# Optimization experiments

Hardware: AMD Instinct MI355X
Metric: run time of the kernel (lower is better)

## Reference

```python
import jax, jax.numpy as jnp
import numpy as np

FACTORS = (16, 8, 8)          # prod == n_embd == 1024
H, DK = 16, 64
FACTOR_PARAMS = tuple(f * (f - 1) // 2 for f in FACTORS)  # (120, 28, 28)
DV = sum(FACTOR_PARAMS)       # 176
DVP = 256                     # next power of two padding
B, T, C = 2, 2048, 1024
OFFSET = 64


def _skew_exp(params, f):
    """params: (..., f*(f-1)//2) -> rotation matrices (..., f, f) via expm of skew-sym."""
    rows, cols = np.triu_indices(f, k=1)
    batch = params.shape[:-1]
    mat = jnp.zeros(batch + (f, f), jnp.float32).at[..., rows, cols].set(params.astype(jnp.float32))
    S = mat - jnp.swapaxes(mat, -1, -2)
    R = jax.vmap(jax.scipy.linalg.expm)(S.reshape((-1, f, f)))
    return R.reshape(batch + (f, f))


def setup_inputs() -> dict:
    key = jax.random.key(0)
    k1, k2, k3, k4, k5 = jax.random.split(key, 5)
    return {
        "x": jax.random.normal(k1, (B, T, C), jnp.float32),
        "cached_k": jax.random.normal(k2, (B, H, OFFSET, DK), jnp.float32),
        "cached_v": jax.random.normal(k3, (B, H, OFFSET, DVP), jnp.float32),
        "W_QK": jax.random.normal(k4, (2 * H * DK, C), jnp.float32) * 0.02,
        "W_V": jax.random.normal(k5, (H * DV, C), jnp.float32) * 0.02,
    }


def reference(x, cached_k, cached_v, W_QK, W_V):
    Bx, Tx, Cx = x.shape
    qk = x @ W_QK.T                                  # (B,T,2*H*DK)
    q, k = jnp.split(qk, 2, axis=-1)
    q = q.reshape(Bx, Tx, H, DK).transpose(0, 2, 1, 3)   # (B,H,T,DK)
    k = k.reshape(Bx, Tx, H, DK).transpose(0, 2, 1, 3)
    v = (x @ W_V.T).reshape(Bx, Tx, H, DV).transpose(0, 2, 1, 3)  # (B,H,T,DV)
    v = jnp.pad(v, ((0, 0), (0, 0), (0, 0), (0, DVP - DV)))       # pad to DVP

    offset = cached_k.shape[2]
    k = jnp.concatenate([cached_k, k], axis=2)       # (B,H,offset+T,DK)
    v = jnp.concatenate([cached_v, v], axis=2)       # (B,H,offset+T,DVP)

    neg_inf = jnp.finfo(jnp.float32).min
    causal = jnp.triu(jnp.full((Tx, Tx), neg_inf, jnp.float32), k=1)
    mask = jnp.concatenate([jnp.zeros((Tx, offset), jnp.float32), causal], axis=1)

    scores = jnp.einsum('bhqd,bhkd->bhqk', q, k) * (1.0 / np.sqrt(DK)) + mask
    attn = jax.nn.softmax(scores, axis=-1)
    rot = jnp.einsum('bhqk,bhkd->bhqd', attn, v)[..., :DV]   # (B,H,T,DV)
    rot = rot.transpose(0, 2, 1, 3).sum(axis=2)              # sum over heads -> (B,T,DV)

    splits = jnp.split(rot, np.cumsum(FACTOR_PARAMS)[:-1].tolist(), axis=-1)
    y = x.reshape(Bx, Tx, *FACTORS)
    for i, (p, f) in enumerate(zip(splits, FACTORS)):
        R = _skew_exp(p, f).astype(x.dtype)          # (B,T,f,f)
        y = jnp.moveaxis(y, 2 + i, 2)
        sh = y.shape
        y = (R @ y.reshape(Bx, Tx, f, -1)).reshape(sh)
        y = jnp.moveaxis(y, 2, 2 + i)
    y = y.reshape(Bx, Tx, Cx)
    return y, k, v
```

## Files before the change

### kernel.cpp

```cpp
#include <hip/hip_runtime.h>

typedef _Float16 h8 __attribute__((ext_vector_type(8)));
typedef _Float16 h4 __attribute__((ext_vector_type(4)));
typedef float f4 __attribute__((ext_vector_type(4)));

#define NB 2
#define NT 2048
#define NC 1024
#define NH 16
#define DKK 64
#define DV 176
#define DVP 256
#define OFF 64
#define KV 2112
#define SCALE_Q 0.18033688011112f
#define CLAMP_S 11.541560327111f

__device__ __forceinline__ void load_lds16(const _Float16* g, _Float16* l) {
    __builtin_amdgcn_global_load_lds(
        (const __attribute__((address_space(1))) void*)g,
        (__attribute__((address_space(3))) void*)l, 16, 0, 0);
}

#define PREPA_X   1048576
#define PREPA_QK  1572864
#define PREPA_WV  2293760
#define PREPA_END 2473984
__global__ __launch_bounds__(256)
void k_prep_a(const float* __restrict__ x, const float* __restrict__ wqk,
              const float* __restrict__ wv, _Float16* __restrict__ xh,
              _Float16* __restrict__ wqkh, _Float16* __restrict__ wvh,
              float* __restrict__ rotb) {
    int i = blockIdx.x * 256 + threadIdx.x;
    if (i >= PREPA_END) return;
    if (i < PREPA_X) {
        float4 v = *(const float4*)(x + (size_t)i * 4);
        h4 h = {(_Float16)v.x, (_Float16)v.y, (_Float16)v.z, (_Float16)v.w};
        *(h4*)(xh + (size_t)i * 4) = h;
    } else if (i < PREPA_QK) {
        int j = i - PREPA_X;
        float4 v = *(const float4*)(wqk + (size_t)j * 4);
        h4 h = {(_Float16)v.x, (_Float16)v.y, (_Float16)v.z, (_Float16)v.w};
        *(h4*)(wqkh + (size_t)j * 4) = h;
    } else if (i < PREPA_WV) {
        int j = i - PREPA_QK;
        float4 v = *(const float4*)(wv + (size_t)j * 4);
        h4 h = {(_Float16)v.x, (_Float16)v.y, (_Float16)v.z, (_Float16)v.w};
        *(h4*)(wvh + (size_t)j * 4) = h;
    } else {
        int j = i - PREPA_WV;
        *(float4*)(rotb + (size_t)j * 4) = (float4){0.f, 0.f, 0.f, 0.f};
    }
}

#define PREPB_CK   32768
#define PREPB_CV   163840
#define PREPB_END  1474560
__global__ __launch_bounds__(256)
void k_prep_b(const float* __restrict__ ck, const float* __restrict__ cv,
              float* __restrict__ out_k, _Float16* __restrict__ kh,
              float* __restrict__ out_v, _Float16* __restrict__ vTh) {
    int i = blockIdx.x * 256 + threadIdx.x;
    if (i >= PREPB_END) return;
    if (i < PREPB_CK) {
        int bh = i >> 10, rem = i & 1023;
        int pos = rem >> 4, d4 = (rem & 15) * 4;
        float4 v = *(const float4*)(ck + (size_t)i * 4);
        size_t o = ((size_t)bh * KV + pos) * DKK + d4;
        *(float4*)(out_k + o) = v;
        h4 h = {(_Float16)v.x, (_Float16)v.y, (_Float16)v.z, (_Float16)v.w};
        *(h4*)(kh + o) = h;
    } else if (i < PREPB_CV) {
        int j = i - PREPB_CK;
        int bh = j >> 12, rem = j & 4095;
        int pos = rem >> 6, c4 = (rem & 63) * 4;
        float4 v = *(const float4*)(cv + (size_t)j * 4);
        *(float4*)(out_v + ((size_t)bh * KV + pos) * DVP + c4) = v;
        if (c4 < DV) {
            _Float16* vt = vTh + ((size_t)bh * DV + c4) * KV + pos;
            vt[0]              = (_Float16)v.x;
            vt[KV]             = (_Float16)v.y;
            vt[2 * (size_t)KV] = (_Float16)v.z;
            vt[3 * (size_t)KV] = (_Float16)v.w;
        }
    } else {
        int j = i - PREPB_CV;
        int bh = j / 40960, rem = j - bh * 40960;
        int t = rem / 20, c4 = DV + (rem - t * 20) * 4;
        *(float4*)(out_v + ((size_t)bh * KV + OFF + t) * DVP + c4) = (float4){0.f, 0.f, 0.f, 0.f};
    }
}

__global__ __launch_bounds__(256)
void k_gemm_fused(const _Float16* __restrict__ xh, const _Float16* __restrict__ wh,
                  _Float16* __restrict__ qh, _Float16* __restrict__ kh,
                  float* __restrict__ out_k, _Float16* __restrict__ vTh,
                  float* __restrict__ out_v) {
    __shared__ char smem_raw[36864];
    auto As = (_Float16(*)[64])smem_raw;
    auto Bs = (_Float16(*)[64])(smem_raw + 16384);
    auto Ts = (_Float16(*)[64][72])smem_raw;

    const int tid = threadIdx.x;
    const int lane = tid & 63, w = tid >> 6;
    const int lr = lane & 15, lg = lane >> 4;
    const int wm = w >> 1, wn = w & 1;
    const int n = blockIdx.x, x = n & 7, idx = n >> 3;
    const int mi = (x & 3) * 8 + idx / 19;
    const int ni = (x >> 2) * 19 + idx % 19;
    const int m0 = mi * 128, n0 = ni * 128;
    const int srow = lane >> 3;
    const int sc16 = (lane & 7) ^ srow;

    f4 acc[4][4];
#pragma unroll
    for (int i = 0; i < 4; i++)
#pragma unroll
        for (int j = 0; j < 4; j++) acc[i][j] = (f4){0.f, 0.f, 0.f, 0.f};

    for (int k0 = 0; k0 < NC; k0 += 64) {
        __syncthreads();
#pragma unroll
        for (int j = 0; j < 4; j++) {
            int i = w * 4 + j;
            int row = i * 8 + srow;
            load_lds16(&xh[(size_t)(m0 + row) * NC + k0 + sc16 * 8],
                       (_Float16*)As + i * 512);
            load_lds16(&wh[(size_t)(n0 + row) * NC + k0 + sc16 * 8],
                       (_Float16*)Bs + i * 512);
        }
        asm volatile("s_waitcnt vmcnt(0)" ::: "memory");
        __syncthreads();

#pragma unroll
        for (int ks = 0; ks < 2; ks++) {
            h8 a[4], b[4];
#pragma unroll
            for (int mt = 0; mt < 4; mt++) {
                int row = wm * 64 + mt * 16 + lr;
                a[mt] = *(const h8*)&As[row][((ks * 4 + lg) ^ (lr & 7)) * 8];
            }
#pragma unroll
            for (int nt = 0; nt < 4; nt++) {
                int row = wn * 64 + nt * 16 + lr;
                b[nt] = *(const h8*)&Bs[row][((ks * 4 + lg) ^ (lr & 7)) * 8];
            }
#pragma unroll
            for (int mt = 0; mt < 4; mt++)
#pragma unroll
                for (int nt = 0; nt < 4; nt++)
                    acc[mt][nt] = __builtin_amdgcn_mfma_f32_16x16x32_f16(a[mt], b[nt], acc[mt][nt], 0, 0, 0);
        }
    }

    if (ni < 8) {
#pragma unroll
        for (int mt = 0; mt < 4; mt++)
#pragma unroll
            for (int nt = 0; nt < 4; nt++)
#pragma unroll
                for (int r = 0; r < 4; r++) {
                    int grow = m0 + wm * 64 + mt * 16 + lg * 4 + r;
                    int gcol = n0 + wn * 64 + nt * 16 + lr;
                    int b_ = grow >> 11, t = grow & (NT - 1);
                    int h = gcol >> 6, dk = gcol & 63;
                    qh[((size_t)(b_ * NH + h) * NT + t) * DKK + dk] =
                        (_Float16)(acc[mt][nt][r] * SCALE_Q);
                }
    } else if (ni < 16) {
#pragma unroll
        for (int mt = 0; mt < 4; mt++)
#pragma unroll
            for (int nt = 0; nt < 4; nt++)
#pragma unroll
                for (int r = 0; r < 4; r++) {
                    int grow = m0 + wm * 64 + mt * 16 + lg * 4 + r;
                    int g2 = n0 - 1024 + wn * 64 + nt * 16 + lr;
                    float v = acc[mt][nt][r];
                    int b_ = grow >> 11, t = grow & (NT - 1);
                    int h = g2 >> 6, dk = g2 & 63;
                    size_t idxk = ((size_t)(b_ * NH + h) * KV + OFF + t) * DKK + dk;
                    out_k[idxk] = v;
                    kh[idxk] = (_Float16)v;
                }
    } else {
        __syncthreads();
#pragma unroll
        for (int mt = 0; mt < 4; mt++)
#pragma unroll
            for (int nt = 0; nt < 4; nt++) {
                h4 ph;
#pragma unroll
                for (int r = 0; r < 4; r++) {
                    int grow = m0 + wm * 64 + mt * 16 + lg * 4 + r;
                    int gcol = n0 - 2048 + wn * 64 + nt * 16 + lr;
                    float v = acc[mt][nt][r];
                    int b_ = grow >> 11, t = grow & (NT - 1);
                    int h = gcol / DV;
                    int c = gcol - h * DV;
                    out_v[((size_t)(b_ * NH + h) * KV + OFF + t) * DVP + c] = v;
                    ph[r] = (_Float16)v;
                }
                *(h4*)&Ts[w][nt * 16 + lr][mt * 16 + lg * 4] = ph;
            }
        __syncthreads();
        {
            const int b_ = m0 >> 11;
            const int mloc = m0 & (NT - 1);
            _Float16* vout = vTh + ((size_t)b_ * (NH * DV) + (n0 - 2048)) * KV + OFF + mloc;
            const int seg = tid & 31;
            const int rr = tid >> 5;
#pragma unroll
            for (int i = 0; i < 16; i++) {
                int c = i * 8 + rr;
                int buf = ((seg >> 4) << 1) | (c >> 6);
                h4 vv = *(const h4*)&Ts[buf][c & 63][(seg & 15) * 4];
                *(h4*)&vout[(size_t)c * KV + seg * 4] = vv;
            }
        }
    }
}

__global__ __launch_bounds__(256, 4)
void k_attn(const _Float16* __restrict__ qh, const _Float16* __restrict__ kh,
            const _Float16* __restrict__ vTh, float* __restrict__ rot) {
    __shared__ _Float16 Ks[64][64];
    __shared__ _Float16 Vs[176][64];
    __shared__ _Float16 Ps[4][16][72];
    const int tid = threadIdx.x, lane = tid & 63, w = tid >> 6;
    const int lr = lane & 15, lg = lane >> 4;
    const int n = blockIdx.x;
    const int gq = 31 - (n >> 5);
    const int bh = (n & 7) + 8 * ((n >> 3) & 3);
    const int b_ = bh >> 4;
    const int qt = gq * 4 + w;
    const int q = qt * 16 + lr;

    const _Float16* qp = qh + ((size_t)bh * NT + q) * DKK;
    h8 bq0 = *(const h8*)(qp + lg * 8);
    h8 bq1 = *(const h8*)(qp + 32 + lg * 8);

    const _Float16* kbase = kh + (size_t)bh * KV * DKK;
    const _Float16* vbase = vTh + (size_t)bh * DV * KV;

    f4 o[11];
#pragma unroll
    for (int i = 0; i < 11; i++) o[i] = (f4){0.f, 0.f, 0.f, 0.f};
    float l_acc = 0.f;

    const int nkt = gq + 2;
    const int srow = lane >> 3, sslot = lane & 7;
    const int sc16 = sslot ^ srow;

    for (int kt = 0; kt < nkt; kt++) {
        __syncthreads();
#pragma unroll
        for (int j = 0; j < 2; j++) {
            int i = w * 2 + j;
            int row = i * 8 + srow;
            load_lds16(&kbase[(size_t)(kt * 64 + row) * DKK + sc16 * 8],
                       (_Float16*)Ks + i * 512);
        }
#pragma unroll
        for (int j = 0; j < 6; j++) {
            int i = w * 6 + j;
            if (i < 22) {
                int row = i * 8 + srow;
                load_lds16(&vbase[(size_t)row * KV + kt * 64 + sc16 * 8],
                           (_Float16*)Vs + i * 512);
            }
        }
        asm volatile("s_waitcnt vmcnt(0)" ::: "memory");
        __syncthreads();

        f4 s[4];
#pragma unroll
        for (int nt = 0; nt < 4; nt++) {
            int krow = nt * 16 + lr;
            h8 ak0 = *(const h8*)&Ks[krow][(lg ^ (lr & 7)) * 8];
            h8 ak1 = *(const h8*)&Ks[krow][((4 + lg) ^ (lr & 7)) * 8];
            f4 st = (f4){0.f, 0.f, 0.f, 0.f};
            st = __builtin_amdgcn_mfma_f32_16x16x32_f16(ak0, bq0, st, 0, 0, 0);
            st = __builtin_amdgcn_mfma_f32_16x16x32_f16(ak1, bq1, st, 0, 0, 0);
            s[nt] = st;
        }

#pragma unroll
        for (int nt = 0; nt < 4; nt++) {
            h4 ph;
#pragma unroll
            for (int r = 0; r < 4; r++) {
                int key = kt * 64 + nt * 16 + lg * 4 + r;
                float sv = fminf(s[nt][r], CLAMP_S);
                float p = (key <= q + OFF) ? __builtin_exp2f(sv) : 0.f;
                l_acc += p;
                ph[r] = (_Float16)p;
            }
            *(h4*)&Ps[w][lr][nt * 16 + lg * 4] = ph;
        }

#pragma unroll
        for (int ks = 0; ks < 2; ks++) {
            h8 ap = *(const h8*)&Ps[w][lr][ks * 32 + lg * 8];
#pragma unroll
            for (int nt = 0; nt < 11; nt++) {
                int vrow = nt * 16 + lr;
                h8 bv = *(const h8*)&Vs[vrow][((ks * 4 + lg) ^ (lr & 7)) * 8];
                o[nt] = __builtin_amdgcn_mfma_f32_16x16x32_f16(ap, bv, o[nt], 0, 0, 0);
            }
        }
    }

    l_acc += __shfl_xor(l_acc, 16);
    l_acc += __shfl_xor(l_acc, 32);
    float lq[4];
#pragma unroll
    for (int r = 0; r < 4; r++) lq[r] = 1.f / __shfl(l_acc, lg * 4 + r);
#pragma unroll
    for (int r = 0; r < 4; r++) {
        int t = qt * 16 + lg * 4 + r;
#pragma unroll
        for (int nt = 0; nt < 11; nt++) {
            atomicAdd(&rot[((size_t)b_ * NT + t) * DV + nt * 16 + lr], o[nt][r] * lq[r]);
        }
    }
}

__device__ __forceinline__ int triu16(int r, int c) { return r * 15 - (r * (r - 1)) / 2 + (c - r - 1); }
__device__ __forceinline__ int triu8(int r, int c)  { return r * 7  - (r * (r - 1)) / 2 + (c - r - 1); }

__global__ __launch_bounds__(64)
void k_rotate(const float* __restrict__ x, const float* __restrict__ rot,
              float* __restrict__ y) {
    __shared__ float A16[16][16], Ta[16][16], Tb[16][16];
    __shared__ float A8[2][8][8], T8a[2][8][8], T8b[2][8][8];
    __shared__ float pbuf[176];
    __shared__ float xt[1024], t1[1024], t2[1024];
    const int tok = blockIdx.x;
    const int lane = threadIdx.x;

    for (int i = lane; i < 176; i += 64) pbuf[i] = rot[(size_t)tok * DV + i];
    for (int i = lane; i < 1024; i += 64) xt[i] = x[(size_t)tok * NC + i];
    __syncthreads();

#pragma unroll
    for (int j = 0; j < 4; j++) {
        int e = lane * 4 + j, r = e >> 4, c = e & 15;
        float v = 0.f;
        if (r < c) v = pbuf[triu16(r, c)];
        else if (r > c) v = -pbuf[triu16(c, r)];
        A16[r][c] = v;
    }
    {
        int r = lane >> 3, c = lane & 7;
#pragma unroll
        for (int m = 0; m < 2; m++) {
            float v = 0.f;
            if (r < c) v = pbuf[120 + m * 28 + triu8(r, c)];
            else if (r > c) v = -pbuf[120 + m * 28 + triu8(c, r)];
            A8[m][r][c] = v;
        }
    }
    __syncthreads();

    float rn = 0.f;
    if (lane < 16) {
#pragma unroll
        for (int c = 0; c < 16; c++) rn += fabsf(A16[lane][c]);
    }
#pragma unroll
    for (int mm = 1; mm < 16; mm <<= 1) rn = fmaxf(rn, __shfl_xor(rn, mm));
    rn = __shfl(rn, 0);
    int s = 0;
    while (rn > 0.5f && s < 60) { rn *= 0.5f; s++; }
    const float sc16 = exp2f((float)(-s));
    __syncthreads();
#pragma unroll
    for (int j = 0; j < 4; j++) { int e = lane * 4 + j; A16[e >> 4][e & 15] *= sc16; }
    __syncthreads();
#pragma unroll
    for (int j = 0; j < 4; j++) {
        int e = lane * 4 + j, r = e >> 4, c = e & 15;
        Ta[r][c] = (r == c ? 1.f : 0.f) + A16[r][c] * (1.f / 12.f);
    }
    __syncthreads();
    float (*Tc)[16] = Ta, (*Tn)[16] = Tb;
    for (int k = 11; k >= 1; k--) {
#pragma unroll
        for (int j = 0; j < 4; j++) {
            int e = lane * 4 + j, r = e >> 4, c = e & 15;
            float acc = 0.f;
#pragma unroll
            for (int q = 0; q < 16; q++) acc += A16[r][q] * Tc[q][c];
            Tn[r][c] = acc * (1.f / (float)k) + (r == c ? 1.f : 0.f);
        }
        __syncthreads();
        float (*tmp)[16] = Tc; Tc = Tn; Tn = tmp;
    }
    for (int it = 0; it < s; it++) {
#pragma unroll
        for (int j = 0; j < 4; j++) {
            int e = lane * 4 + j, r = e >> 4, c = e & 15;
            float acc = 0.f;
#pragma unroll
            for (int q = 0; q < 16; q++) acc += Tc[r][q] * Tc[q][c];
            Tn[r][c] = acc;
        }
        __syncthreads();
        float (*tmp)[16] = Tc; Tc = Tn; Tn = tmp;
    }

    float (*R2p)[8] = T8a[0];
    float (*R3p)[8] = T8a[1];
    {
        int r = lane >> 3, c = lane & 7;
        for (int m = 0; m < 2; m++) {
            float rn8 = 0.f;
            if (lane < 8) {
#pragma unroll
                for (int cc = 0; cc < 8; cc++) rn8 += fabsf(A8[m][lane][cc]);
            }
#pragma unroll
            for (int mm = 1; mm < 8; mm <<= 1) rn8 = fmaxf(rn8, __shfl_xor(rn8, mm));
            rn8 = __shfl(rn8, 0);
            int s8 = 0;
            while (rn8 > 0.5f && s8 < 60) { rn8 *= 0.5f; s8++; }
            float sc8 = exp2f((float)(-s8));
            __syncthreads();
            A8[m][r][c] *= sc8;
            __syncthreads();
            T8a[m][r][c] = (r == c ? 1.f : 0.f) + A8[m][r][c] * (1.f / 12.f);
            __syncthreads();
            float (*tc)[8] = T8a[m], (*tn)[8] = T8b[m];
            for (int k = 11; k >= 1; k--) {
                float acc = 0.f;
#pragma unroll
                for (int q = 0; q < 8; q++) acc += A8[m][r][q] * tc[q][c];
                tn[r][c] = acc * (1.f / (float)k) + (r == c ? 1.f : 0.f);
                __syncthreads();
                float (*tmp)[8] = tc; tc = tn; tn = tmp;
            }
            for (int it = 0; it < s8; it++) {
                float acc = 0.f;
#pragma unroll
                for (int q = 0; q < 8; q++) acc += tc[r][q] * tc[q][c];
                tn[r][c] = acc;
                __syncthreads();
                float (*tmp)[8] = tc; tc = tn; tn = tmp;
            }
            if (m == 0) R2p = tc; else R3p = tc;
        }
    }
    __syncthreads();

    for (int o = lane; o < 1024; o += 64) {
        int c = o & 7, base = o & ~7;
        float acc = 0.f;
#pragma unroll
        for (int j = 0; j < 8; j++) acc += R3p[c][j] * xt[base + j];
        t1[o] = acc;
    }
    __syncthreads();
    for (int o = lane; o < 1024; o += 64) {
        int c = o & 7, bb = (o >> 3) & 7, a = o >> 6;
        float acc = 0.f;
#pragma unroll
        for (int j = 0; j < 8; j++) acc += R2p[bb][j] * t1[a * 64 + j * 8 + c];
        t2[o] = acc;
    }
    __syncthreads();
    for (int o = lane; o < 1024; o += 64) {
        int rr = o & 63, a = o >> 6;
        float acc = 0.f;
#pragma unroll
        for (int j = 0; j < 16; j++) acc += Tc[a][j] * t2[j * 64 + rr];
        y[(size_t)tok * NC + o] = acc;
    }
}

extern "C" void kernel_launch(void* const* d_in, const int* in_sizes, int n_in,
                              void* d_out, int out_size, void* d_ws, size_t ws_size,
                              hipStream_t stream) {
    const float* x   = (const float*)d_in[0];
    const float* ck  = (const float*)d_in[1];
    const float* cv  = (const float*)d_in[2];
    const float* wqk = (const float*)d_in[3];
    const float* wv  = (const float*)d_in[4];

    float* out_y = (float*)d_out;
    float* out_k = out_y + (size_t)NB * NT * NC;
    float* out_v = out_k + (size_t)NB * NH * KV * DKK;

    char* ws = (char*)d_ws;
    _Float16* xh   = (_Float16*)ws;  ws += (size_t)NB * NT * NC * 2;
    _Float16* wqkh = (_Float16*)ws;  ws += (size_t)2 * NH * DKK * NC * 2;
    _Float16* wvh  = (_Float16*)ws;  ws += (size_t)NH * DV * NC * 2;
    _Float16* qh   = (_Float16*)ws;  ws += (size_t)NB * NH * NT * DKK * 2;
    _Float16* kh   = (_Float16*)ws;  ws += (size_t)NB * NH * KV * DKK * 2;
    _Float16* vTh  = (_Float16*)ws;  ws += (size_t)NB * NH * DV * KV * 2;
    float*    rotb = (float*)ws;     ws += (size_t)NB * NT * DV * 4;

    k_prep_a<<<dim3((PREPA_END + 255) / 256), dim3(256), 0, stream>>>(
        x, wqk, wv, xh, wqkh, wvh, rotb);
    k_prep_b<<<dim3((PREPB_END + 255) / 256), dim3(256), 0, stream>>>(
        ck, cv, out_k, kh, out_v, vTh);

    k_gemm_fused<<<dim3(1216), dim3(256), 0, stream>>>(xh, wqkh, qh, kh, out_k, vTh, out_v);

    k_attn<<<dim3(1024), dim3(256), 0, stream>>>(qh, kh, vTh, rotb);

    k_rotate<<<dim3(NB * NT), dim3(64), 0, stream>>>(x, rotb, out_y);
}
```

Before: 200.4 us.

## Stage Q/K fp16 epilogue through LDS and overlap K-score compute with V loads

In the fused projection GEMM, the fp16 Q and K outputs are now written to an LDS tile first, then stored to global memory as coalesced 16-byte vectors instead of scattered 2-byte stores. The fp32 K output is still stored directly. In the attention loop, the wait before computing scores now only covers the K tile, so the QK MFMAs and softmax overlap the remaining V tile loads. A second wait and barrier are added before the PV product. This trades extra barriers and an LDS round-trip for better store coalescing and more load/compute overlap.

```diff
diff --git a/kernel.cpp b/kernel.cpp
--- a/kernel.cpp
+++ b/kernel.cpp
@@ -100,6 +100,7 @@
     auto As = (_Float16(*)[64])smem_raw;
     auto Bs = (_Float16(*)[64])(smem_raw + 16384);
     auto Ts = (_Float16(*)[64][72])smem_raw;
+    auto Tq = (_Float16(*)[128][68])smem_raw;
 
     const int tid = threadIdx.x;
     const int lane = tid & 63, w = tid >> 6;
@@ -153,36 +154,54 @@
         }
     }
 
+    const int b_ = m0 >> 11;
+    const int mloc = m0 & (NT - 1);
+
     if (ni < 8) {
+        __syncthreads();
 #pragma unroll
         for (int mt = 0; mt < 4; mt++)
 #pragma unroll
             for (int nt = 0; nt < 4; nt++)
 #pragma unroll
+                for (int r = 0; r < 4; r++)
+                    Tq[wn][wm * 64 + mt * 16 + lg * 4 + r][nt * 16 + lr] =
+                        (_Float16)(acc[mt][nt][r] * SCALE_Q);
+        __syncthreads();
+        const int h0 = n0 >> 6;
+#pragma unroll
+        for (int i = 0; i < 8; i++) {
+            int id = i * 256 + tid;
+            int hh = id >> 10, rem = id & 1023;
+            int t = rem >> 3, dk8 = (rem & 7) * 8;
+            h8 v = *(const h8*)&Tq[hh][t][dk8];
+            *(h8*)&qh[((size_t)(b_ * NH + h0 + hh) * NT + mloc + t) * DKK + dk8] = v;
+        }
+    } else if (ni < 16) {
+        __syncthreads();
+#pragma unroll
+        for (int mt = 0; mt < 4; mt++)
+#pragma unroll
+            for (int nt = 0; nt < 4; nt++)
+#pragma unroll
                 for (int r = 0; r < 4; r++) {
-                    int grow = m0 + wm * 64 + mt * 16 + lg * 4 + r;
-                    int gcol = n0 + wn * 64 + nt * 16 + lr;
-                    int b_ = grow >> 11, t = grow & (NT - 1);
-                    int h = gcol >> 6, dk = gcol & 63;
-                    qh[((size_t)(b_ * NH + h) * NT + t) * DKK + dk] =
-                        (_Float16)(acc[mt][nt][r] * SCALE_Q);
-                }
-    } else if (ni < 16) {
-#pragma unroll
-        for (int mt = 0; mt < 4; mt++)
-#pragma unroll
-            for (int nt = 0; nt < 4; nt++)
-#pragma unroll
-                for (int r = 0; r < 4; r++) {
-                    int grow = m0 + wm * 64 + mt * 16 + lg * 4 + r;
+                    int t = wm * 64 + mt * 16 + lg * 4 + r;
                     int g2 = n0 - 1024 + wn * 64 + nt * 16 + lr;
                     float v = acc[mt][nt][r];
-                    int b_ = grow >> 11, t = grow & (NT - 1);
                     int h = g2 >> 6, dk = g2 & 63;
-                    size_t idxk = ((size_t)(b_ * NH + h) * KV + OFF + t) * DKK + dk;
-                    out_k[idxk] = v;
-                    kh[idxk] = (_Float16)v;
+                    out_k[((size_t)(b_ * NH + h) * KV + OFF + mloc + t) * DKK + dk] = v;
+                    Tq[wn][t][nt * 16 + lr] = (_Float16)v;
                 }
+        __syncthreads();
+        const int h0 = (n0 - 1024) >> 6;
+#pragma unroll
+        for (int i = 0; i < 8; i++) {
+            int id = i * 256 + tid;
+            int hh = id >> 10, rem = id & 1023;
+            int t = rem >> 3, dk8 = (rem & 7) * 8;
+            h8 v = *(const h8*)&Tq[hh][t][dk8];
+            *(h8*)&kh[((size_t)(b_ * NH + h0 + hh) * KV + OFF + mloc + t) * DKK + dk8] = v;
+        }
     } else {
         __syncthreads();
 #pragma unroll
@@ -195,18 +214,16 @@
                     int grow = m0 + wm * 64 + mt * 16 + lg * 4 + r;
                     int gcol = n0 - 2048 + wn * 64 + nt * 16 + lr;
                     float v = acc[mt][nt][r];
-                    int b_ = grow >> 11, t = grow & (NT - 1);
+                    int bb = grow >> 11, t = grow & (NT - 1);
                     int h = gcol / DV;
                     int c = gcol - h * DV;
-                    out_v[((size_t)(b_ * NH + h) * KV + OFF + t) * DVP + c] = v;
+                    out_v[((size_t)(bb * NH + h) * KV + OFF + t) * DVP + c] = v;
                     ph[r] = (_Float16)v;
                 }
                 *(h4*)&Ts[w][nt * 16 + lr][mt * 16 + lg * 4] = ph;
             }
         __syncthreads();
         {
-            const int b_ = m0 >> 11;
-            const int mloc = m0 & (NT - 1);
             _Float16* vout = vTh + ((size_t)b_ * (NH * DV) + (n0 - 2048)) * KV + OFF + mloc;
             const int seg = tid & 31;
             const int rr = tid >> 5;
@@ -270,7 +287,7 @@
                            (_Float16*)Vs + i * 512);
             }
         }
-        asm volatile("s_waitcnt vmcnt(0)" ::: "memory");
+        asm volatile("s_waitcnt vmcnt(4)" ::: "memory");
         __syncthreads();
 
         f4 s[4];
@@ -298,6 +315,9 @@
             }
             *(h4*)&Ps[w][lr][nt * 16 + lg * 4] = ph;
         }
+
+        asm volatile("s_waitcnt vmcnt(0)" ::: "memory");
+        __syncthreads();
 
 #pragma unroll
         for (int ks = 0; ks < 2; ks++) {
```

After: 204.2 us. About the same (+1.9%).
